# Kernel tuning notes

Measured on AMD Instinct MI355X. Metric: run time of the kernel, lower is better.

Reference implementation:

```python
import jax, jax.numpy as jnp
import numpy as np

NU, NI = 100000, 50000      # global embedding table sizes
U, I = 50000, 20000         # nodes in this subgraph
E = 400000                  # edges per direction
HID, H = 512, 8
D = HID // H                # out_feats per head = 64
NEG_SLOPE = 0.2


def setup_inputs() -> dict:
    key = jax.random.key(0)
    ks = jax.random.split(key, 16)
    s = 1.0 / np.sqrt(HID)
    a = 1.0 / np.sqrt(D)
    return {
        'u_gid': jax.random.randint(ks[0], (U,), 0, NU),
        'i_gid': jax.random.randint(ks[1], (I,), 0, NI),
        'src_u': jax.random.randint(ks[2], (E,), 0, U),
        'dst_i': jax.random.randint(ks[3], (E,), 0, I),
        'user_emb': jax.random.normal(ks[4], (NU, HID), jnp.float32) * 0.02,
        'item_emb': jax.random.normal(ks[5], (NI, HID), jnp.float32) * 0.02,
        # 'interact' (user -> item) GATConv params
        'W_ui': jax.random.normal(ks[6], (HID, HID), jnp.float32) * s,
        'al_ui': jax.random.normal(ks[7], (H, D), jnp.float32) * a,
        'ar_ui': jax.random.normal(ks[8], (H, D), jnp.float32) * a,
        'b_ui': jnp.zeros((HID,), jnp.float32),
        # 'interact_rev' (item -> user) GATConv params
        'W_iu': jax.random.normal(ks[9], (HID, HID), jnp.float32) * s,
        'al_iu': jax.random.normal(ks[10], (H, D), jnp.float32) * a,
        'ar_iu': jax.random.normal(ks[11], (H, D), jnp.float32) * a,
        'b_iu': jnp.zeros((HID,), jnp.float32),
    }


def gat_conv(h_src, h_dst, src, dst, W, attn_l, attn_r, bias, n_dst):
    """DGL GATConv (eval mode, allow_zero_in_degree): [n_dst, H, D]."""
    fs = (h_src @ W).reshape(-1, H, D)            # [Ns,H,D]
    fd = (h_dst @ W).reshape(-1, H, D)            # [Nd,H,D]
    el = jnp.sum(fs * attn_l, axis=-1)            # [Ns,H]
    er = jnp.sum(fd * attn_r, axis=-1)            # [Nd,H]
    e = jax.nn.leaky_relu(el[src] + er[dst], NEG_SLOPE)   # [E,H]
    # segment softmax over incoming edges of each destination
    emax = jax.ops.segment_max(e, dst, num_segments=n_dst)[dst]
    ex = jnp.exp(e - emax)                        # [E,H]
    denom = jax.ops.segment_sum(ex, dst, num_segments=n_dst)[dst]
    alpha = ex / denom                            # [E,H]
    msg = fs[src] * alpha[:, :, None]             # [E,H,D]
    out = jax.ops.segment_sum(msg, dst, num_segments=n_dst)  # zero for isolated dst
    return out + bias.reshape(1, H, D)


def reference(u_gid, i_gid, src_u, dst_i, user_emb, item_emb,
              W_ui, al_ui, ar_ui, b_ui, W_iu, al_iu, ar_iu, b_iu):
    h_u0 = user_emb[u_gid]                        # [U,HID]
    h_i0 = item_emb[i_gid]                        # [I,HID]
    # 'interact': user -> item
    h_item = gat_conv(h_u0, h_i0, src_u, dst_i, W_ui, al_ui, ar_ui, b_ui, I)
    # 'interact_rev': item -> user (reversed edges)
    h_user = gat_conv(h_i0, h_u0, dst_i, src_u, W_iu, al_iu, ar_iu, b_iu, U)
    h_user = h_user.reshape(U, HID)
    h_item = h_item.reshape(I, HID)
    item_mean = jnp.mean(h_item, axis=0, keepdims=True)        # [1,HID]
    item_expand = jnp.broadcast_to(item_mean, (U, HID))
    return jnp.concatenate([h_user, item_expand], axis=1)      # [U, 2*HID]
```

## Files before the change

### kernel.cpp

```cpp
#include <hip/hip_runtime.h>
#include <hip/hip_bf16.h>
#include <stdint.h>

#define U_NODES 50000
#define I_NODES 20000
#define N_NODES 70000
#define M_PAD   70016
#define E_EDGES 400000
#define HID     512

typedef __attribute__((ext_vector_type(8))) short short8;
typedef __attribute__((ext_vector_type(4))) float floatx4;

static __device__ __forceinline__ uint16_t f2b(float f) {
    uint32_t x = __float_as_uint(f);
    x += 0x7fffu + ((x >> 16) & 1u);
    return (uint16_t)(x >> 16);
}
static __device__ __forceinline__ float b2f(short u) {
    return __uint_as_float(((uint32_t)(uint16_t)u) << 16);
}

__global__ void gather_cast(const int* __restrict__ u_gid, const int* __restrict__ i_gid,
                            const float* __restrict__ user_emb, const float* __restrict__ item_emb,
                            uint16_t* __restrict__ Xb)
{
    int t = blockIdx.x * 256 + threadIdx.x;
    int n = t >> 7;
    int j = (t & 127) << 2;
    uint2 o;
    if (n < N_NODES) {
        const float* src = (n < U_NODES) ? (user_emb + (size_t)u_gid[n] * HID)
                                         : (item_emb + (size_t)i_gid[n - U_NODES] * HID);
        float4 v = *(const float4*)(src + j);
        o.x = (uint32_t)f2b(v.x) | ((uint32_t)f2b(v.y) << 16);
        o.y = (uint32_t)f2b(v.z) | ((uint32_t)f2b(v.w) << 16);
    } else { o.x = 0u; o.y = 0u; }
    *(uint2*)(Xb + (size_t)n * HID + j) = o;
}

__global__ void prep_w(const float* __restrict__ Wui, const float* __restrict__ Wiu,
                       uint16_t* __restrict__ Wt)
{
    int t = blockIdx.x * 256 + threadIdx.x;
    int n = t >> 9, k = t & 511;
    float v = (n < 512) ? Wui[k * 512 + n] : Wiu[k * 512 + (n - 512)];
    Wt[(size_t)n * 512 + k] = f2b(v);
}

__global__ __launch_bounds__(256) void gemm_bf16(const uint16_t* __restrict__ Xb,
                                                 const uint16_t* __restrict__ Wt,
                                                 const float* __restrict__ al_ui, const float* __restrict__ ar_ui,
                                                 const float* __restrict__ al_iu, const float* __restrict__ ar_iu,
                                                 uint16_t* __restrict__ F,
                                                 float* __restrict__ ELui, float* __restrict__ ERui,
                                                 float* __restrict__ ELiu, float* __restrict__ ERiu)
{
    __shared__ __align__(16) uint16_t As[3][128 * 32];
    __shared__ __align__(16) uint16_t Bs[3][128 * 32];
    const int tid = threadIdx.x;
    const int wave = tid >> 6, lane = tid & 63;

    int bid = blockIdx.x;
    int x = bid & 7, ii = bid >> 3;
    int L = x * 547 + ii;
    const int m0 = (L >> 3) * 128;
    const int n0 = (L & 7) * 128;
    const int wm = (wave & 1) * 64;
    const int wn = (wave >> 1) * 64;

    const int rl2 = lane >> 2;
    const int sg = ((lane & 3) ^ ((lane >> 3) & 3)) * 8;
    const int ca = wave * 2, cb = wave * 2 + 1;
    const uint16_t* gA0 = Xb + (size_t)(m0 + ca * 16 + rl2) * HID + sg;
    const uint16_t* gA1 = Xb + (size_t)(m0 + cb * 16 + rl2) * HID + sg;
    const uint16_t* gB0 = Wt + (size_t)(n0 + ca * 16 + rl2) * HID + sg;
    const uint16_t* gB1 = Wt + (size_t)(n0 + cb * 16 + rl2) * HID + sg;

    floatx4 zero = {0.f, 0.f, 0.f, 0.f};
    floatx4 acc[4][4];
    #pragma unroll
    for (int a = 0; a < 4; ++a)
        #pragma unroll
        for (int b = 0; b < 4; ++b) acc[a][b] = zero;

    const int r = lane & 15, quad = lane >> 4;
    const int slq8 = (quad ^ ((r >> 1) & 3)) * 8;

#define STAGE(KO, BUF) do {                                                                         \
    __builtin_amdgcn_global_load_lds((const __attribute__((address_space(1))) void*)(gA0 + (KO)),   \
                                     (__attribute__((address_space(3))) void*)(&As[BUF][ca * 512]), 16, 0, 0); \
    __builtin_amdgcn_global_load_lds((const __attribute__((address_space(1))) void*)(gA1 + (KO)),   \
                                     (__attribute__((address_space(3))) void*)(&As[BUF][cb * 512]), 16, 0, 0); \
    __builtin_amdgcn_global_load_lds((const __attribute__((address_space(1))) void*)(gB0 + (KO)),   \
                                     (__attribute__((address_space(3))) void*)(&Bs[BUF][ca * 512]), 16, 0, 0); \
    __builtin_amdgcn_global_load_lds((const __attribute__((address_space(1))) void*)(gB1 + (KO)),   \
                                     (__attribute__((address_space(3))) void*)(&Bs[BUF][cb * 512]), 16, 0, 0); \
} while (0)

#define COMPUTE(BUF) do {                                                                           \
    short8 af[4], bf[4];                                                                            \
    _Pragma("unroll")                                                                               \
    for (int tm = 0; tm < 4; ++tm)                                                                  \
        af[tm] = *(const short8*)&As[BUF][(wm + tm * 16 + r) * 32 + slq8];                          \
    _Pragma("unroll")                                                                               \
    for (int tn = 0; tn < 4; ++tn)                                                                  \
        bf[tn] = *(const short8*)&Bs[BUF][(wn + tn * 16 + r) * 32 + slq8];                          \
    _Pragma("unroll")                                                                               \
    for (int tm = 0; tm < 4; ++tm)                                                                  \
        _Pragma("unroll")                                                                           \
        for (int tn = 0; tn < 4; ++tn)                                                              \
            acc[tm][tn] = __builtin_amdgcn_mfma_f32_16x16x32_bf16(af[tm], bf[tn], acc[tm][tn], 0, 0, 0); \
} while (0)

    STAGE(0, 0);
    STAGE(32, 1);
    #pragma unroll
    for (int t = 0; t < 15; ++t) {
        asm volatile("s_waitcnt vmcnt(4)");
        __builtin_amdgcn_sched_barrier(0);
        __builtin_amdgcn_s_barrier();
        __builtin_amdgcn_sched_barrier(0);
        if (t < 14) STAGE((t + 2) * 32, (t + 2) % 3);
        COMPUTE(t % 3);
    }
    asm volatile("s_waitcnt vmcnt(0)");
    __builtin_amdgcn_sched_barrier(0);
    __builtin_amdgcn_s_barrier();
    __builtin_amdgcn_sched_barrier(0);
    COMPUTE(0);

#undef STAGE
#undef COMPUTE

    const bool collo = (n0 < 512);
    const bool allU = (m0 + 128 <= U_NODES);
    const bool allI = (m0 >= U_NODES);
    const bool storeb = (allU && collo) || (allI && !collo) || (!allU && !allI);

    const int colh = n0 + wn;
    const int h = (colh & 511) >> 6;
    const float* arv = collo ? ar_ui : ar_iu;
    float* ERp = collo ? ERui : ERiu;
    float ar4[4];
    #pragma unroll
    for (int tn = 0; tn < 4; ++tn) ar4[tn] = arv[h * 64 + tn * 16 + r];

    if (storeb) {
        const float* alv = collo ? al_ui : al_iu;
        float* ELp = collo ? ELui : ELiu;
        float al4[4];
        #pragma unroll
        for (int tn = 0; tn < 4; ++tn) al4[tn] = alv[h * 64 + tn * 16 + r];
        #pragma unroll
        for (int tm = 0; tm < 4; ++tm) {
            #pragma unroll
            for (int rr = 0; rr < 4; ++rr) {
                int row = m0 + wm + tm * 16 + quad * 4 + rr;
                float sl = 0.f, sr = 0.f;
                #pragma unroll
                for (int tn = 0; tn < 4; ++tn) {
                    sl += acc[tm][tn][rr] * al4[tn];
                    sr += acc[tm][tn][rr] * ar4[tn];
                }
                if (row < N_NODES && ((row < U_NODES) == collo)) {
                    #pragma unroll
                    for (int tn = 0; tn < 4; ++tn) {
                        int col = n0 + wn + tn * 16 + r;
                        F[(size_t)row * 1024 + col] = f2b(acc[tm][tn][rr]);
                    }
                }
                #pragma unroll
                for (int d = 1; d < 16; d <<= 1) {
                    sl += __shfl_xor(sl, d);
                    sr += __shfl_xor(sr, d);
                }
                if (r == 0 && row < N_NODES) {
                    ELp[row * 8 + h] = sl;
                    ERp[row * 8 + h] = sr;
                }
            }
        }
    } else {
        #pragma unroll
        for (int tm = 0; tm < 4; ++tm) {
            #pragma unroll
            for (int rr = 0; rr < 4; ++rr) {
                int row = m0 + wm + tm * 16 + quad * 4 + rr;
                float sr = 0.f;
                #pragma unroll
                for (int tn = 0; tn < 4; ++tn) sr += acc[tm][tn][rr] * ar4[tn];
                #pragma unroll
                for (int d = 1; d < 16; d <<= 1) sr += __shfl_xor(sr, d);
                if (r == 0 && row < N_NODES) ERp[row * 8 + h] = sr;
            }
        }
    }
}

__global__ void hist_kernel(const int* __restrict__ src_u, const int* __restrict__ dst_i,
                            int* __restrict__ counts_i, int* __restrict__ counts_u)
{
    int e = blockIdx.x * 256 + threadIdx.x;
    if (e >= E_EDGES) return;
    atomicAdd(&counts_i[dst_i[e]], 1);
    atomicAdd(&counts_u[src_u[e]], 1);
}

#define SCAN_CHUNK 1024
#define IBLKS ((I_NODES + SCAN_CHUNK - 1) / SCAN_CHUNK)
#define UBLKS ((U_NODES + SCAN_CHUNK - 1) / SCAN_CHUNK)

__global__ __launch_bounds__(256) void scan_level1(const int* __restrict__ counts_i,
                                                   const int* __restrict__ counts_u,
                                                   int* __restrict__ bsum)
{
    int b = blockIdx.x, t = threadIdx.x;
    const int* cnt; int n, base;
    if (b < IBLKS) { cnt = counts_i; n = I_NODES; base = b * SCAN_CHUNK; }
    else           { cnt = counts_u; n = U_NODES; base = (b - IBLKS) * SCAN_CHUNK; }
    int idx = base + t * 4;
    int s = 0;
    #pragma unroll
    for (int k = 0; k < 4; ++k) { int i = idx + k; if (i < n) s += cnt[i]; }
    __shared__ int ws[4];
    int lane = t & 63, w = t >> 6;
    int xv = s;
    #pragma unroll
    for (int d = 1; d < 64; d <<= 1) xv += __shfl_xor(xv, d);
    if (lane == 0) ws[w] = xv;
    __syncthreads();
    if (t == 0) bsum[b] = ws[0] + ws[1] + ws[2] + ws[3];
}

__global__ __launch_bounds__(256) void scan_level3(const int* __restrict__ counts_i,
                                                   const int* __restrict__ counts_u,
                                                   const int* __restrict__ bsum,
                                                   int* __restrict__ offs_i, int* __restrict__ cur_i,
                                                   int* __restrict__ offs_u, int* __restrict__ cur_u)
{
    int b = blockIdx.x, t = threadIdx.x;
    const int* cnt; int n, base, segfirst, seglast; int* offs; int* cur;
    if (b < IBLKS) { cnt = counts_i; n = I_NODES; base = b * SCAN_CHUNK; segfirst = 0; seglast = IBLKS - 1; offs = offs_i; cur = cur_i; }
    else           { cnt = counts_u; n = U_NODES; base = (b - IBLKS) * SCAN_CHUNK; segfirst = IBLKS; seglast = IBLKS + UBLKS - 1; offs = offs_u; cur = cur_u; }
    int lane = t & 63, w = t >> 6;

    __shared__ int s_boff;
    __shared__ int ws[4];
    if (w == 0) {
        int i = segfirst + lane;
        int v = (i < b) ? bsum[i] : 0;
        #pragma unroll
        for (int d = 1; d < 64; d <<= 1) v += __shfl_xor(v, d);
        if (lane == 0) s_boff = v;
    }

    int idx = base + t * 4;
    int v4[4]; int s = 0;
    #pragma unroll
    for (int k = 0; k < 4; ++k) { int i = idx + k; v4[k] = (i < n) ? cnt[i] : 0; s += v4[k]; }
    int xv = s;
    #pragma unroll
    for (int d = 1; d < 64; d <<= 1) { int y = __shfl_up(xv, d, 64); if (lane >= d) xv += y; }
    if (lane == 63) ws[w] = xv;
    __syncthreads();
    int wexcl = 0;
    #pragma unroll
    for (int k = 0; k < 4; ++k) if (k < w) wexcl += ws[k];
    int excl = s_boff + wexcl + (xv - s);
    #pragma unroll
    for (int k = 0; k < 4; ++k) {
        int i = idx + k;
        if (i < n) { offs[i] = excl; cur[i] = excl; }
        excl += v4[k];
    }
    if (t == 0 && b == seglast)
        offs[n] = s_boff + ws[0] + ws[1] + ws[2] + ws[3];
}

__global__ void scatter_kernel(const int* __restrict__ src_u, const int* __restrict__ dst_i,
                               int* __restrict__ cur_i, int* __restrict__ cur_u,
                               int* __restrict__ sorted_ui, int* __restrict__ sorted_iu)
{
    int e = blockIdx.x * 256 + threadIdx.x;
    if (e >= E_EDGES) return;
    int s = src_u[e], d = dst_i[e];
    int p = atomicAdd(&cur_i[d], 1);
    int q = atomicAdd(&cur_u[s], 1);
    sorted_ui[p] = s;
    sorted_iu[q] = U_NODES + d;
}

#define IBLK ((I_NODES + 3) / 4)
#define UBLK ((U_NODES + 3) / 4)
__global__ __launch_bounds__(256) void agg3_kernel(
    const int* __restrict__ offs_i, const int* __restrict__ sorted_ui,
    const int* __restrict__ offs_u, const int* __restrict__ sorted_iu,
    const float* __restrict__ ELui, const float* __restrict__ ERui,
    const float* __restrict__ ELiu, const float* __restrict__ ERiu,
    const uint16_t* __restrict__ F, const float* __restrict__ b_iu,
    float* __restrict__ out, float* __restrict__ itemF)
{
    int bid = blockIdx.x;
    int w = threadIdx.x >> 6, lane = threadIdx.x & 63;
    bool item_mode = bid < IBLK;
    const int* offs; const int* srcs; const float* el_tab; const float* er_tab;
    int dst, colbase, n_dst, dstnode;
    if (item_mode) {
        offs = offs_i; srcs = sorted_ui; el_tab = ELui; er_tab = ERui;
        dst = bid * 4 + w; colbase = 0; n_dst = I_NODES;
        dstnode = U_NODES + dst;
    } else {
        offs = offs_u; srcs = sorted_iu; el_tab = ELiu; er_tab = ERiu;
        dst = (bid - IBLK) * 4 + w; colbase = 512; n_dst = U_NODES;
        dstnode = dst;
    }
    if (dst >= n_dst) return;
    int h = lane >> 3;
    int j0 = offs[dst], j1 = offs[dst + 1];
    float er_h = er_tab[dstnode * 8 + h];

    float den = 0.f;
    float acc[8] = {0.f, 0.f, 0.f, 0.f, 0.f, 0.f, 0.f, 0.f};
    const int fb = colbase + lane * 8;
    int j = j0;
    for (; j + 8 <= j1; j += 8) {
        int s[8]; float wt[8]; short8 f[8];
        #pragma unroll
        for (int i = 0; i < 8; ++i) s[i] = srcs[j + i];
        #pragma unroll
        for (int i = 0; i < 8; ++i) {
            float e0 = el_tab[s[i] * 8 + h] + er_h;
            e0 = (e0 >= 0.f) ? e0 : 0.2f * e0;
            wt[i] = __expf(e0);
        }
        #pragma unroll
        for (int i = 0; i < 8; ++i) f[i] = *(const short8*)&F[(size_t)s[i] * 1024 + fb];
        #pragma unroll
        for (int i = 0; i < 8; ++i) {
            den += wt[i];
            #pragma unroll
            for (int q = 0; q < 8; ++q) acc[q] += wt[i] * b2f(f[i][q]);
        }
    }
    for (; j + 4 <= j1; j += 4) {
        int s[4]; float wt[4]; short8 f[4];
        #pragma unroll
        for (int i = 0; i < 4; ++i) s[i] = srcs[j + i];
        #pragma unroll
        for (int i = 0; i < 4; ++i) {
            float e0 = el_tab[s[i] * 8 + h] + er_h;
            e0 = (e0 >= 0.f) ? e0 : 0.2f * e0;
            wt[i] = __expf(e0);
        }
        #pragma unroll
        for (int i = 0; i < 4; ++i) f[i] = *(const short8*)&F[(size_t)s[i] * 1024 + fb];
        #pragma unroll
        for (int i = 0; i < 4; ++i) {
            den += wt[i];
            #pragma unroll
            for (int q = 0; q < 8; ++q) acc[q] += wt[i] * b2f(f[i][q]);
        }
    }
    for (; j < j1; ++j) {
        int s0 = srcs[j];
        float e0 = el_tab[s0 * 8 + h] + er_h;
        e0 = (e0 >= 0.f) ? e0 : 0.2f * e0;
        float w0 = __expf(e0);
        short8 f0 = *(const short8*)&F[(size_t)s0 * 1024 + fb];
        den += w0;
        #pragma unroll
        for (int q = 0; q < 8; ++q) acc[q] += w0 * b2f(f0[q]);
    }
    float inv = (j1 > j0) ? (1.f / den) : 0.f;
    #pragma unroll
    for (int q = 0; q < 8; ++q) acc[q] *= inv;

    int col = lane * 8;
    if (item_mode) {
        float* o = itemF + (size_t)dst * 512 + col;
        floatx4 v0 = {acc[0], acc[1], acc[2], acc[3]};
        floatx4 v1 = {acc[4], acc[5], acc[6], acc[7]};
        __builtin_nontemporal_store(v0, (floatx4*)(o + 0));
        __builtin_nontemporal_store(v1, (floatx4*)(o + 4));
    } else {
        float* o = out + (size_t)dst * 1024 + col;
        floatx4 v0 = {acc[0] + b_iu[col + 0], acc[1] + b_iu[col + 1],
                      acc[2] + b_iu[col + 2], acc[3] + b_iu[col + 3]};
        floatx4 v1 = {acc[4] + b_iu[col + 4], acc[5] + b_iu[col + 5],
                      acc[6] + b_iu[col + 6], acc[7] + b_iu[col + 7]};
        __builtin_nontemporal_store(v0, (floatx4*)(o + 0));
        __builtin_nontemporal_store(v1, (floatx4*)(o + 4));
    }
}

__global__ void item_reduce(const float* __restrict__ itemF, float* __restrict__ partial2)
{
    int b = blockIdx.x;
    int t = threadIdx.x;
    int cg = (t & 127) * 4;
    int rp = t >> 7;
    float4 s = {0.f, 0.f, 0.f, 0.f};
    int r0 = b * 125;
    for (int r = r0 + rp; r < r0 + 125; r += 2) {
        float4 v = *(const float4*)&itemF[(size_t)r * 512 + cg];
        s.x += v.x; s.y += v.y; s.z += v.z; s.w += v.w;
    }
    *(float4*)&partial2[(size_t)(b * 2 + rp) * 512 + cg] = s;
}

__global__ void meanvec_kernel(const float* __restrict__ partial2, const float* __restrict__ b_ui,
                               float* __restrict__ mean_vec)
{
    int c = threadIdx.x;
    float s = 0.f;
    for (int p = 0; p < 320; ++p) s += partial2[p * 512 + c];
    mean_vec[c] = s * (1.0f / (float)I_NODES) + b_ui[c];
}

__global__ void bcast_kernel(const float* __restrict__ mean_vec, float* __restrict__ out)
{
    int t = blockIdx.x * 256 + threadIdx.x;
    int u = t >> 7, q = t & 127;
    floatx4 v = ((const floatx4*)mean_vec)[q];
    __builtin_nontemporal_store(v, (floatx4*)(out + (size_t)u * 1024 + 512 + q * 4));
}

extern "C" void kernel_launch(void* const* d_in, const int* in_sizes, int n_in,
                              void* d_out, int out_size, void* d_ws, size_t ws_size,
                              hipStream_t stream)
{
    const int*   u_gid    = (const int*)d_in[0];
    const int*   i_gid    = (const int*)d_in[1];
    const int*   src_u    = (const int*)d_in[2];
    const int*   dst_i    = (const int*)d_in[3];
    const float* user_emb = (const float*)d_in[4];
    const float* item_emb = (const float*)d_in[5];
    const float* W_ui     = (const float*)d_in[6];
    const float* al_ui    = (const float*)d_in[7];
    const float* ar_ui    = (const float*)d_in[8];
    const float* b_ui     = (const float*)d_in[9];
    const float* W_iu     = (const float*)d_in[10];
    const float* al_iu    = (const float*)d_in[11];
    const float* ar_iu    = (const float*)d_in[12];
    const float* b_iu     = (const float*)d_in[13];
    float* out = (float*)d_out;

    char* ws = (char*)d_ws;
    size_t off = 0;
    auto alloc = [&](size_t bytes) -> void* {
        void* p = ws + off;
        off = (off + bytes + 255) & ~(size_t)255;
        return p;
    };
    uint16_t* Xb   = (uint16_t*)alloc((size_t)M_PAD * 512 * 2);
    uint16_t* Wt   = (uint16_t*)alloc((size_t)1024 * 512 * 2);
    uint16_t* F    = (uint16_t*)alloc((size_t)M_PAD * 1024 * 2);
    float* ELui    = (float*)alloc((size_t)N_NODES * 8 * 4);
    float* ERui    = (float*)alloc((size_t)N_NODES * 8 * 4);
    float* ELiu    = (float*)alloc((size_t)N_NODES * 8 * 4);
    float* ERiu    = (float*)alloc((size_t)N_NODES * 8 * 4);
    int* offs_i    = (int*)alloc((size_t)(I_NODES + 1) * 4);
    int* cur_i     = (int*)alloc((size_t)I_NODES * 4);
    int* offs_u    = (int*)alloc((size_t)(U_NODES + 1) * 4);
    int* cur_u     = (int*)alloc((size_t)U_NODES * 4);
    int* sorted_ui = (int*)alloc((size_t)E_EDGES * 4);
    int* sorted_iu = (int*)alloc((size_t)E_EDGES * 4);
    int* bsum      = (int*)alloc((size_t)(IBLKS + UBLKS) * 4);
    float* itemF   = (float*)alloc((size_t)I_NODES * 512 * 4);
    float* partial2= (float*)alloc((size_t)320 * 512 * 4);
    char* zptr = ws + off;
    int*   counts_i = (int*)alloc((size_t)I_NODES * 4);
    int*   counts_u = (int*)alloc((size_t)U_NODES * 4);
    size_t zbytes = (size_t)((ws + off) - zptr);
    float* mean_vec = (float*)alloc(512 * 4);
    (void)ws_size; (void)in_sizes; (void)n_in; (void)out_size;

    hipMemsetAsync(zptr, 0, zbytes, stream);
    prep_w<<<2048, 256, 0, stream>>>(W_ui, W_iu, Wt);
    gather_cast<<<M_PAD * 128 / 256, 256, 0, stream>>>(u_gid, i_gid, user_emb, item_emb, Xb);
    gemm_bf16<<<(M_PAD / 128) * 8, 256, 0, stream>>>(Xb, Wt, al_ui, ar_ui, al_iu, ar_iu,
                                                     F, ELui, ERui, ELiu, ERiu);
    hist_kernel<<<(E_EDGES + 255) / 256, 256, 0, stream>>>(src_u, dst_i, counts_i, counts_u);
    scan_level1<<<IBLKS + UBLKS, 256, 0, stream>>>(counts_i, counts_u, bsum);
    scan_level3<<<IBLKS + UBLKS, 256, 0, stream>>>(counts_i, counts_u, bsum,
                                                   offs_i, cur_i, offs_u, cur_u);
    scatter_kernel<<<(E_EDGES + 255) / 256, 256, 0, stream>>>(src_u, dst_i, cur_i, cur_u,
                                                              sorted_ui, sorted_iu);
    agg3_kernel<<<IBLK + UBLK, 256, 0, stream>>>(offs_i, sorted_ui, offs_u, sorted_iu,
                                                 ELui, ERui, ELiu, ERiu,
                                                 F, b_iu, out, itemF);
    item_reduce<<<160, 256, 0, stream>>>(itemF, partial2);
    meanvec_kernel<<<1, 512, 0, stream>>>(partial2, b_ui, mean_vec);
    bcast_kernel<<<U_NODES * 128 / 256, 256, 0, stream>>>(mean_vec, out);
}
```

Before: 756.9 us.

## Widen GEMM tile to 128x256 with double-buffered LDS pipeline

Enlarges the projection GEMM output tile from 128x128 to 128x256, giving each wave 4x8 MFMA accumulators and two heads per epilogue. The aim is more operand reuse per LDS load and half as many blocks re-reading the A tile. The 3-stage pipeline with explicit vmcnt waits becomes a 2-stage double buffer synchronised with __syncthreads. The block remap is reworked for 547x4 blocks. The costs are higher register pressure (128 accumulator floats per lane), possibly lower occupancy, and less latency hiding with only two buffers.

```diff
diff --git a/kernel.cpp b/kernel.cpp
--- a/kernel.cpp
+++ b/kernel.cpp
@@ -56,79 +56,82 @@
                                                  float* __restrict__ ELui, float* __restrict__ ERui,
                                                  float* __restrict__ ELiu, float* __restrict__ ERiu)
 {
-    __shared__ __align__(16) uint16_t As[3][128 * 32];
-    __shared__ __align__(16) uint16_t Bs[3][128 * 32];
+    __shared__ __align__(16) uint16_t As[2][128 * 32];
+    __shared__ __align__(16) uint16_t Bs[2][256 * 32];
     const int tid = threadIdx.x;
     const int wave = tid >> 6, lane = tid & 63;
 
     int bid = blockIdx.x;
-    int x = bid & 7, ii = bid >> 3;
-    int L = x * 547 + ii;
-    const int m0 = (L >> 3) * 128;
-    const int n0 = (L & 7) * 128;
+    int x = bid & 7, i8 = bid >> 3;
+    int L = x * 273 + ((x < 4) ? x : 4) + i8;
+    const int m0 = (L >> 2) * 128;
+    const int n0 = (L & 3) * 256;
     const int wm = (wave & 1) * 64;
-    const int wn = (wave >> 1) * 64;
+    const int wn = (wave >> 1) * 128;
 
     const int rl2 = lane >> 2;
     const int sg = ((lane & 3) ^ ((lane >> 3) & 3)) * 8;
-    const int ca = wave * 2, cb = wave * 2 + 1;
-    const uint16_t* gA0 = Xb + (size_t)(m0 + ca * 16 + rl2) * HID + sg;
-    const uint16_t* gA1 = Xb + (size_t)(m0 + cb * 16 + rl2) * HID + sg;
-    const uint16_t* gB0 = Wt + (size_t)(n0 + ca * 16 + rl2) * HID + sg;
-    const uint16_t* gB1 = Wt + (size_t)(n0 + cb * 16 + rl2) * HID + sg;
+    const uint16_t* gp[6];
+    uint16_t* lp0[6];
+    uint16_t* lp1[6];
+    #pragma unroll
+    for (int l = 0; l < 6; ++l) {
+        int cc = wave * 6 + l;
+        if (cc < 8) {
+            gp[l]  = Xb + (size_t)(m0 + cc * 16 + rl2) * HID + sg;
+            lp0[l] = &As[0][cc * 512];
+            lp1[l] = &As[1][cc * 512];
+        } else {
+            int cb2 = cc - 8;
+            gp[l]  = Wt + (size_t)(n0 + cb2 * 16 + rl2) * HID + sg;
+            lp0[l] = &Bs[0][cb2 * 512];
+            lp1[l] = &Bs[1][cb2 * 512];
+        }
+    }
 
     floatx4 zero = {0.f, 0.f, 0.f, 0.f};
-    floatx4 acc[4][4];
+    floatx4 acc[4][8];
     #pragma unroll
     for (int a = 0; a < 4; ++a)
         #pragma unroll
-        for (int b = 0; b < 4; ++b) acc[a][b] = zero;
+        for (int b = 0; b < 8; ++b) acc[a][b] = zero;
 
     const int r = lane & 15, quad = lane >> 4;
     const int slq8 = (quad ^ ((r >> 1) & 3)) * 8;
 
 #define STAGE(KO, BUF) do {                                                                         \
-    __builtin_amdgcn_global_load_lds((const __attribute__((address_space(1))) void*)(gA0 + (KO)),   \
-                                     (__attribute__((address_space(3))) void*)(&As[BUF][ca * 512]), 16, 0, 0); \
-    __builtin_amdgcn_global_load_lds((const __attribute__((address_space(1))) void*)(gA1 + (KO)),   \
-                                     (__attribute__((address_space(3))) void*)(&As[BUF][cb * 512]), 16, 0, 0); \
-    __builtin_amdgcn_global_load_lds((const __attribute__((address_space(1))) void*)(gB0 + (KO)),   \
-                                     (__attribute__((address_space(3))) void*)(&Bs[BUF][ca * 512]), 16, 0, 0); \
-    __builtin_amdgcn_global_load_lds((const __attribute__((address_space(1))) void*)(gB1 + (KO)),   \
-                                     (__attribute__((address_space(3))) void*)(&Bs[BUF][cb * 512]), 16, 0, 0); \
+    _Pragma("unroll")                                                                               \
+    for (int l = 0; l < 6; ++l) {                                                                   \
+        uint16_t* d = (BUF) ? lp1[l] : lp0[l];                                                      \
+        __builtin_amdgcn_global_load_lds((const __attribute__((address_space(1))) void*)(gp[l] + (KO)), \
+                                         (__attribute__((address_space(3))) void*)d, 16, 0, 0);     \
+    }                                                                                               \
 } while (0)
 
 #define COMPUTE(BUF) do {                                                                           \
-    short8 af[4], bf[4];                                                                            \
+    short8 af[4], bf[8];                                                                            \
     _Pragma("unroll")                                                                               \
     for (int tm = 0; tm < 4; ++tm)                                                                  \
         af[tm] = *(const short8*)&As[BUF][(wm + tm * 16 + r) * 32 + slq8];                          \
     _Pragma("unroll")                                                                               \
-    for (int tn = 0; tn < 4; ++tn)                                                                  \
+    for (int tn = 0; tn < 8; ++tn)                                                                  \
         bf[tn] = *(const short8*)&Bs[BUF][(wn + tn * 16 + r) * 32 + slq8];                          \
     _Pragma("unroll")                                                                               \
     for (int tm = 0; tm < 4; ++tm)                                                                  \
         _Pragma("unroll")                                                                           \
-        for (int tn = 0; tn < 4; ++tn)                                                              \
+        for (int tn = 0; tn < 8; ++tn)                                                              \
             acc[tm][tn] = __builtin_amdgcn_mfma_f32_16x16x32_bf16(af[tm], bf[tn], acc[tm][tn], 0, 0, 0); \
 } while (0)
 
     STAGE(0, 0);
-    STAGE(32, 1);
+    __syncthreads();
     #pragma unroll
     for (int t = 0; t < 15; ++t) {
-        asm volatile("s_waitcnt vmcnt(4)");
-        __builtin_amdgcn_sched_barrier(0);
-        __builtin_amdgcn_s_barrier();
-        __builtin_amdgcn_sched_barrier(0);
-        if (t < 14) STAGE((t + 2) * 32, (t + 2) % 3);
-        COMPUTE(t % 3);
-    }
-    asm volatile("s_waitcnt vmcnt(0)");
-    __builtin_amdgcn_sched_barrier(0);
-    __builtin_amdgcn_s_barrier();
-    __builtin_amdgcn_sched_barrier(0);
-    COMPUTE(0);
+        STAGE((t + 1) * 32, (t + 1) & 1);
+        COMPUTE(t & 1);
+        __syncthreads();
+    }
+    COMPUTE(1);
 
 #undef STAGE
 #undef COMPUTE
@@ -138,46 +141,55 @@
     const bool allI = (m0 >= U_NODES);
     const bool storeb = (allU && collo) || (allI && !collo) || (!allU && !allI);
 
-    const int colh = n0 + wn;
-    const int h = (colh & 511) >> 6;
+    const int cb = (n0 + wn) & 511;
+    const int h0 = cb >> 6, h1 = h0 + 1;
     const float* arv = collo ? ar_ui : ar_iu;
     float* ERp = collo ? ERui : ERiu;
-    float ar4[4];
-    #pragma unroll
-    for (int tn = 0; tn < 4; ++tn) ar4[tn] = arv[h * 64 + tn * 16 + r];
+    float ar8[8];
+    #pragma unroll
+    for (int tn = 0; tn < 8; ++tn) ar8[tn] = arv[cb + tn * 16 + r];
 
     if (storeb) {
         const float* alv = collo ? al_ui : al_iu;
         float* ELp = collo ? ELui : ELiu;
-        float al4[4];
-        #pragma unroll
-        for (int tn = 0; tn < 4; ++tn) al4[tn] = alv[h * 64 + tn * 16 + r];
+        float al8[8];
+        #pragma unroll
+        for (int tn = 0; tn < 8; ++tn) al8[tn] = alv[cb + tn * 16 + r];
         #pragma unroll
         for (int tm = 0; tm < 4; ++tm) {
             #pragma unroll
             for (int rr = 0; rr < 4; ++rr) {
                 int row = m0 + wm + tm * 16 + quad * 4 + rr;
-                float sl = 0.f, sr = 0.f;
+                float slA = 0.f, srA = 0.f, slB = 0.f, srB = 0.f;
                 #pragma unroll
                 for (int tn = 0; tn < 4; ++tn) {
-                    sl += acc[tm][tn][rr] * al4[tn];
-                    sr += acc[tm][tn][rr] * ar4[tn];
+                    slA += acc[tm][tn][rr] * al8[tn];
+                    srA += acc[tm][tn][rr] * ar8[tn];
+                }
+                #pragma unroll
+                for (int tn = 4; tn < 8; ++tn) {
+                    slB += acc[tm][tn][rr] * al8[tn];
+                    srB += acc[tm][tn][rr] * ar8[tn];
                 }
                 if (row < N_NODES && ((row < U_NODES) == collo)) {
                     #pragma unroll
-                    for (int tn = 0; tn < 4; ++tn) {
+                    for (int tn = 0; tn < 8; ++tn) {
                         int col = n0 + wn + tn * 16 + r;
                         F[(size_t)row * 1024 + col] = f2b(acc[tm][tn][rr]);
                     }
                 }
                 #pragma unroll
                 for (int d = 1; d < 16; d <<= 1) {
-                    sl += __shfl_xor(sl, d);
-                    sr += __shfl_xor(sr, d);
+                    slA += __shfl_xor(slA, d);
+                    srA += __shfl_xor(srA, d);
+                    slB += __shfl_xor(slB, d);
+                    srB += __shfl_xor(srB, d);
                 }
                 if (r == 0 && row < N_NODES) {
-                    ELp[row * 8 + h] = sl;
-                    ERp[row * 8 + h] = sr;
+                    ELp[row * 8 + h0] = slA;
+                    ERp[row * 8 + h0] = srA;
+                    ELp[row * 8 + h1] = slB;
+                    ERp[row * 8 + h1] = srB;
                 }
             }
         }
@@ -187,12 +199,20 @@
             #pragma unroll
             for (int rr = 0; rr < 4; ++rr) {
                 int row = m0 + wm + tm * 16 + quad * 4 + rr;
-                float sr = 0.f;
+                float srA = 0.f, srB = 0.f;
                 #pragma unroll
-                for (int tn = 0; tn < 4; ++tn) sr += acc[tm][tn][rr] * ar4[tn];
+                for (int tn = 0; tn < 4; ++tn) srA += acc[tm][tn][rr] * ar8[tn];
                 #pragma unroll
-                for (int d = 1; d < 16; d <<= 1) sr += __shfl_xor(sr, d);
-                if (r == 0 && row < N_NODES) ERp[row * 8 + h] = sr;
+                for (int tn = 4; tn < 8; ++tn) srB += acc[tm][tn][rr] * ar8[tn];
+                #pragma unroll
+                for (int d = 1; d < 16; d <<= 1) {
+                    srA += __shfl_xor(srA, d);
+                    srB += __shfl_xor(srB, d);
+                }
+                if (r == 0 && row < N_NODES) {
+                    ERp[row * 8 + h0] = srA;
+                    ERp[row * 8 + h1] = srB;
+                }
             }
         }
     }
@@ -479,8 +499,8 @@
     hipMemsetAsync(zptr, 0, zbytes, stream);
     prep_w<<<2048, 256, 0, stream>>>(W_ui, W_iu, Wt);
     gather_cast<<<M_PAD * 128 / 256, 256, 0, stream>>>(u_gid, i_gid, user_emb, item_emb, Xb);
-    gemm_bf16<<<(M_PAD / 128) * 8, 256, 0, stream>>>(Xb, Wt, al_ui, ar_ui, al_iu, ar_iu,
-                                                     F, ELui, ERui, ELiu, ERiu);
+    gemm_bf16<<<547 * 4, 256, 0, stream>>>(Xb, Wt, al_ui, ar_ui, al_iu, ar_iu,
+                                           F, ELui, ERui, ELiu, ERiu);
     hist_kernel<<<(E_EDGES + 255) / 256, 256, 0, stream>>>(src_u, dst_i, counts_i, counts_u);
     scan_level1<<<IBLKS + UBLKS, 256, 0, stream>>>(counts_i, counts_u, bsum);
     scan_level3<<<IBLKS + UBLKS, 256, 0, stream>>>(counts_i, counts_u, bsum,
```

Result: slower. 807.2 us (+6.7%).
